# Kernel optimization log

Measured on AMD Instinct MI355X. Metric: run time of the kernel, lower is better.

The kernel has to match this reference:

```python
import jax, jax.numpy as jnp
import numpy as np

B, T, IN_DIM, OUT_DIM, H = 2, 256, 512, 256, 8
TEMP = 1.0
BN_EPS = 1e-5


def _boundary_mask(bnd):
    # bnd: (B, T) float in {0,1}. Vectorized version of the nested-loop
    # construction: mask[j,k] = prod_{m=min(j,k)..max(j,k)} (1 - bnd[m]), diag=1.
    q = 1.0 - bnd  # (B, T)
    ar = jnp.arange(T)

    def per_batch(qb):
        def row(j):
            # cumprod of q starting at position j (entries before j treated as 1)
            return jnp.cumprod(jnp.where(ar >= j, qb, 1.0))
        M = jax.vmap(row)(ar)                 # (T, T); valid for k >= j
        upper = ar[None, :] >= ar[:, None]
        full = jnp.where(upper, M, M.T)       # symmetrize
        eye = ar[None, :] == ar[:, None]
        return jnp.where(eye, 1.0, full)      # diagonal forced to 1

    return jax.vmap(per_batch)(q)             # (B, T, T)


def setup_inputs() -> dict:
    key = jax.random.key(0)
    ks = jax.random.split(key, 8)
    s_in = 1.0 / np.sqrt(IN_DIM)
    s_hin = 1.0 / np.sqrt(H * IN_DIM)
    return {
        "x": jax.random.normal(ks[0], (B, T, IN_DIM), dtype=jnp.float32),
        "boundary": jax.random.randint(ks[1], (B, T), 0, 2, dtype=jnp.int32),
        "att_proj_w": jax.random.normal(ks[2], (OUT_DIM, IN_DIM), dtype=jnp.float32) * s_in,
        "att_proj_b": jnp.zeros((OUT_DIM,), dtype=jnp.float32),
        "att_weight": jax.random.normal(ks[3], (OUT_DIM, H), dtype=jnp.float32) * (1.0 / np.sqrt(OUT_DIM)),
        "proj_att_w": jax.random.normal(ks[4], (OUT_DIM, H * IN_DIM), dtype=jnp.float32) * s_hin,
        "proj_att_b": jnp.zeros((OUT_DIM,), dtype=jnp.float32),
        "proj_noatt_w": jax.random.normal(ks[5], (OUT_DIM, IN_DIM), dtype=jnp.float32) * s_in,
        "proj_noatt_b": jnp.zeros((OUT_DIM,), dtype=jnp.float32),
        "bn_gamma": jnp.ones((OUT_DIM,), dtype=jnp.float32),
        "bn_beta": jnp.zeros((OUT_DIM,), dtype=jnp.float32),
    }


def reference(x, boundary, att_proj_w, att_proj_b, att_weight,
              proj_att_w, proj_att_b, proj_noatt_w, proj_noatt_b,
              bn_gamma, bn_beta):
    bnd = boundary.astype(x.dtype)

    # pairwise node products: (B, T, T, IN_DIM)
    pm = x[:, :, None, :] * x[:, None, :, :]
    # attention logits: tanh(Linear) @ att_weight -> (B, T, T, H)
    a = jnp.tanh(jnp.einsum('bjkd,od->bjko', pm, att_proj_w) + att_proj_b)
    att = jnp.einsum('bjko,oh->bjkh', a, att_weight) / TEMP

    # boundary message-control mask, then softmax over the key-node axis (dim=-2)
    mask = _boundary_mask(bnd)                 # (B, T, T)
    att = att * mask[..., None]
    att = jax.nn.softmax(att, axis=-2)

    # aggregate per head; torch flattens (IN_DIM, H) -> IN_DIM*H with d-major order
    x1 = jnp.einsum('bjkh,bkd->bjdh', att, x).reshape(x.shape[0], x.shape[1], -1)
    x1 = x1 @ proj_att_w.T + proj_att_b
    x2 = x @ proj_noatt_w.T + proj_noatt_b
    y = x1 + x2                                # (B, T, OUT_DIM)

    # BatchNorm1d in training mode over flattened (B*T, OUT_DIM), biased variance
    flat = y.reshape(-1, y.shape[-1])
    mu = flat.mean(axis=0)
    var = flat.var(axis=0)
    yn = (flat - mu) * jax.lax.rsqrt(var + BN_EPS) * bn_gamma + bn_beta
    return jax.nn.selu(yn.reshape(y.shape))
```

## Files before the change

### kernel.cpp

```cpp
#include <hip/hip_runtime.h>
#include <hip/hip_bf16.h>

#define B_ 2
#define T_ 256
#define D_ 512
#define O_ 256
#define H_ 8

typedef __attribute__((ext_vector_type(4))) float f32x4;
typedef __attribute__((ext_vector_type(8))) short bf16x8;
typedef unsigned short u16;
typedef unsigned int u32;

__device__ __forceinline__ u16 f2b(float f) {
    u32 u = __builtin_bit_cast(u32, f);
    u32 r = (u + 0x7FFFu + ((u >> 16) & 1u)) >> 16;
    return (u16)r;
}
__device__ __forceinline__ u32 cvtpk(float lo, float hi) {
    u32 r;
    asm("v_cvt_pk_bf16_f32 %0, %1, %2" : "=v"(r) : "v"(lo), "v"(hi));
    return r;
}
__device__ __forceinline__ float fast_tanh(float x) {
    float ax = fabsf(x);
    float e = __expf(-2.f * ax);
    float r = (1.f - e) / (1.f + e);
    return x < 0.f ? -r : r;
}
__device__ __forceinline__ uint4 ld8f2b(const float* __restrict__ p) {
    f32x4 a = *reinterpret_cast<const f32x4*>(p);
    f32x4 b = *reinterpret_cast<const f32x4*>(p + 4);
    uint4 pk;
    pk.x = cvtpk(a[0], a[1]);
    pk.y = cvtpk(a[2], a[3]);
    pk.z = cvtpk(b[0], b[1]);
    pk.w = cvtpk(b[2], b[3]);
    return pk;
}
__device__ __forceinline__ void gload16(const void* g, void* l) {
    __builtin_amdgcn_global_load_lds(
        (const __attribute__((address_space(1))) unsigned int*)g,
        (__attribute__((address_space(3))) unsigned int*)l, 16, 0, 0);
}

__global__ void k0_prep(const float* __restrict__ x, const float* __restrict__ W2,
                        const int* __restrict__ bnd,
                        u16* __restrict__ Xbf, u16* __restrict__ W2t,
                        int* __restrict__ scan_g) {
    const int tid = threadIdx.x;
    if (blockIdx.x < 64) {
        int base = (blockIdx.x * 256 + tid) * 16;
        uint4 o0 = ld8f2b(x + base);
        uint4 o1 = ld8f2b(x + base + 8);
        *reinterpret_cast<uint4*>(Xbf + base) = o0;
        *reinterpret_cast<uint4*>(Xbf + base + 8) = o1;
        return;
    }
    if (blockIdx.x >= 192) {
        const int b = blockIdx.x - 192;
        __shared__ int sc[256];
        sc[tid] = bnd[b * 256 + tid];
        __syncthreads();
        for (int off = 1; off < 256; off <<= 1) {
            int v = (tid >= off) ? sc[tid - off] : 0;
            __syncthreads();
            sc[tid] += v;
            __syncthreads();
        }
        scan_g[b * 256 + tid] = sc[tid];
        return;
    }
    const int bx2 = blockIdx.x - 64;
    const int o0 = (bx2 >> 3) * 16;
    const int dc = bx2 & 7;
    __shared__ u16 TL[8192];
    #pragma unroll
    for (int c = 0; c < 8; ++c) {
        int i = tid * 32 + c * 4;
        int r = i >> 9, rem = i & 511;
        f32x4 v = *reinterpret_cast<const f32x4*>(
            W2 + (size_t)(o0 + r) * 4096 + dc * 512 + rem);
        int dd = rem >> 3, h0 = rem & 7;
        TL[(h0 + 0) * 1024 + r * 64 + dd] = f2b(v[0]);
        TL[(h0 + 1) * 1024 + r * 64 + dd] = f2b(v[1]);
        TL[(h0 + 2) * 1024 + r * 64 + dd] = f2b(v[2]);
        TL[(h0 + 3) * 1024 + r * 64 + dd] = f2b(v[3]);
    }
    __syncthreads();
    #pragma unroll
    for (int c = 0; c < 4; ++c) {
        int jj = tid * 32 + c * 8;
        int h = jj >> 10, r = (jj >> 6) & 15, dd = jj & 63;
        *reinterpret_cast<uint4*>(W2t + (size_t)(h * 256 + o0 + r) * 512 + dc * 64 + dd) =
            *reinterpret_cast<const uint4*>(&TL[jj]);
    }
}

__launch_bounds__(256, 4)
__global__ void k1a_att(const u16* __restrict__ Xbf, const float* __restrict__ xf,
                        const float* __restrict__ Wap, const float* __restrict__ bap,
                        const float* __restrict__ aw, float* __restrict__ attpart)
{
    const int oc = blockIdx.x & 3;
    const int j = (blockIdx.x >> 2) & 255;
    const int b = blockIdx.x >> 10;
    const int jt = j >> 6;
    const int tid = threadIdx.x;
    const int w = tid >> 6;
    const int l = tid & 63;
    const int l15 = l & 15;
    const int lgp = l >> 4;
    const bool act = (w >= jt);

    __shared__ __align__(16) u16 XL[256 * 64];
    __shared__ __align__(16) u16 WL[64 * 64];

    const u16* xb = Xbf + b * (T_ * D_);
    const float* xjp = xf + (b * T_ + j) * D_;

    bf16x8 bwreg[2];
    #pragma unroll
    for (int ds = 0; ds < 2; ++ds) {
        u16 awtmp[8];
        #pragma unroll
        for (int e = 0; e < 8; ++e)
            awtmp[e] = (l15 < 8) ? f2b(aw[(oc * 64 + ds * 32 + lgp * 8 + e) * 8 + l15]) : (u16)0;
        bwreg[ds] = *reinterpret_cast<const bf16x8*>(awtmp);
    }

    const int srow_off = (l >> 3);
    const int scol = ((l & 7) ^ ((l >> 3) & 7)) * 8;
    const int i0 = jt * 2;
    const int wr0 = tid >> 3, wsc = (tid & 7) * 8;
    const int wswz0 = ((tid & 7) ^ (wr0 & 7)) * 8;

    f32x4 acc[4][4] = {};
    for (int d0 = 0; d0 < D_; d0 += 64) {
        __syncthreads();
        #pragma unroll
        for (int i = 0; i < 8; ++i) {
            if (i >= i0) {
                int row = i * 32 + w * 8 + srow_off;
                gload16(xb + row * 512 + d0 + scol, &XL[i * 2048 + w * 512]);
            }
        }
        {
            f32x4 xa = *reinterpret_cast<const f32x4*>(xjp + d0 + wsc);
            f32x4 xc = *reinterpret_cast<const f32x4*>(xjp + d0 + wsc + 4);
            const float* wp0 = Wap + (size_t)(oc * 64 + wr0) * 512 + d0 + wsc;
            f32x4 va = *reinterpret_cast<const f32x4*>(wp0);
            f32x4 vb = *reinterpret_cast<const f32x4*>(wp0 + 4);
            uint4 pk;
            pk.x = cvtpk(va[0] * xa[0], va[1] * xa[1]);
            pk.y = cvtpk(va[2] * xa[2], va[3] * xa[3]);
            pk.z = cvtpk(vb[0] * xc[0], vb[1] * xc[1]);
            pk.w = cvtpk(vb[2] * xc[2], vb[3] * xc[3]);
            *reinterpret_cast<uint4*>(&WL[wr0 * 64 + wswz0]) = pk;
            const float* wp1 = wp0 + 32 * 512;
            va = *reinterpret_cast<const f32x4*>(wp1);
            vb = *reinterpret_cast<const f32x4*>(wp1 + 4);
            pk.x = cvtpk(va[0] * xa[0], va[1] * xa[1]);
            pk.y = cvtpk(va[2] * xa[2], va[3] * xa[3]);
            pk.z = cvtpk(vb[0] * xc[0], vb[1] * xc[1]);
            pk.w = cvtpk(vb[2] * xc[2], vb[3] * xc[3]);
            *reinterpret_cast<uint4*>(&WL[(wr0 + 32) * 64 + wswz0]) = pk;
        }
        __syncthreads();
        if (act) {
            #pragma unroll
            for (int ds = 0; ds < 2; ++ds) {
                bf16x8 wfr[4];
                #pragma unroll
                for (int ot = 0; ot < 4; ++ot) {
                    int wc = ((ds * 4 + lgp) ^ (l15 & 7)) * 8;
                    wfr[ot] = *reinterpret_cast<const bf16x8*>(&WL[(ot * 16 + l15) * 64 + wc]);
                }
                #pragma unroll
                for (int kt = 0; kt < 4; ++kt) {
                    int row = w * 64 + kt * 16 + l15;
                    int c16 = ((ds * 4 + lgp) ^ (l15 & 7)) * 8;
                    bf16x8 xfr = *reinterpret_cast<const bf16x8*>(&XL[row * 64 + c16]);
                    #pragma unroll
                    for (int ot = 0; ot < 4; ++ot)
                        acc[ot][kt] = __builtin_amdgcn_mfma_f32_16x16x32_bf16(wfr[ot], xfr, acc[ot][kt], 0, 0, 0);
                }
            }
        }
    }
    u16* a_lds = XL;
    if (act) {
        #pragma unroll
        for (int ot = 0; ot < 4; ++ot) {
            f32x4 bv = *reinterpret_cast<const f32x4*>(bap + oc * 64 + ot * 16 + lgp * 4);
            #pragma unroll
            for (int kt = 0; kt < 4; ++kt) {
                int k = w * 64 + kt * 16 + l15;
                float t0 = fast_tanh(acc[ot][kt][0] + bv[0]);
                float t1 = fast_tanh(acc[ot][kt][1] + bv[1]);
                float t2 = fast_tanh(acc[ot][kt][2] + bv[2]);
                float t3 = fast_tanh(acc[ot][kt][3] + bv[3]);
                uint2 pk;
                pk.x = cvtpk(t0, t1);
                pk.y = cvtpk(t2, t3);
                int c16 = (ot * 2 + (lgp >> 1)) ^ (l15 & 7);
                *reinterpret_cast<uint2*>(&a_lds[k * 64 + c16 * 8 + (lgp & 1) * 4]) = pk;
            }
        }
    }
    f32x4 attacc[4] = {};
    if (act) {
        #pragma unroll
        for (int ds = 0; ds < 2; ++ds) {
            #pragma unroll
            for (int kt = 0; kt < 4; ++kt) {
                int row = w * 64 + kt * 16 + l15;
                int c16 = ((ds * 4 + lgp) ^ (l15 & 7)) * 8;
                bf16x8 af = *reinterpret_cast<const bf16x8*>(&a_lds[row * 64 + c16]);
                attacc[kt] = __builtin_amdgcn_mfma_f32_16x16x32_bf16(af, bwreg[ds], attacc[kt], 0, 0, 0);
            }
        }
        float* dst = attpart + ((size_t)blockIdx.x) * 256 * 8;
        #pragma unroll
        for (int kt = 0; kt < 4; ++kt) {
            if (l15 < 8) {
                #pragma unroll
                for (int i = 0; i < 4; ++i) {
                    int k = w * 64 + kt * 16 + lgp * 4 + i;
                    dst[k * 8 + l15] = attacc[kt][i];
                }
            }
        }
        if (w > jt && l15 < 8) {
            #pragma unroll
            for (int kt = 0; kt < 4; ++kt) {
                #pragma unroll
                for (int i = 0; i < 4; ++i) {
                    int k = w * 64 + kt * 16 + lgp * 4 + i;
                    attpart[(((size_t)(b * 256 + k)) * 4 + oc) * 2048 + j * 8 + l15] = attacc[kt][i];
                }
            }
        }
    }
}

__global__ void k1b_sm(const float* __restrict__ attpart, const int* __restrict__ scan_g,
                       u16* __restrict__ P2)
{
    const int b = blockIdx.x >> 8;
    const int j = blockIdx.x & 255;
    const int tid = threadIdx.x;

    __shared__ float attL[256 * 9];
    __shared__ float maskv[256];

    {
        int k = tid;
        const int* sg = scan_g + b * 256;
        float m;
        if (k == j) m = 1.f;
        else if (k > j) m = ((sg[k] - (j ? sg[j - 1] : 0)) == 0) ? 1.f : 0.f;
        else m = ((sg[j] - (k ? sg[k - 1] : 0)) == 0) ? 1.f : 0.f;
        maskv[k] = m;
    }
    {
        const float* base = attpart + ((size_t)(b * 256 + j) * 4) * 256 * 8 + tid * 8;
        f32x4 s0 = *reinterpret_cast<const f32x4*>(base);
        f32x4 s1 = *reinterpret_cast<const f32x4*>(base + 4);
        #pragma unroll
        for (int oc = 1; oc < 4; ++oc) {
            s0 += *reinterpret_cast<const f32x4*>(base + (size_t)oc * 2048);
            s1 += *reinterpret_cast<const f32x4*>(base + (size_t)oc * 2048 + 4);
        }
        #pragma unroll
        for (int e = 0; e < 4; ++e) attL[tid * 9 + e] = s0[e];
        #pragma unroll
        for (int e = 0; e < 4; ++e) attL[tid * 9 + 4 + e] = s1[e];
    }
    __syncthreads();

    {
        int h = tid >> 5, c = tid & 31;
        float lgv[8];
        float mx = -3.4e38f;
        #pragma unroll
        for (int kk = 0; kk < 8; ++kk) {
            int k = c + kk * 32;
            float v = attL[k * 9 + h] * maskv[k];
            lgv[kk] = v;
            mx = fmaxf(mx, v);
        }
        #pragma unroll
        for (int off = 1; off < 32; off <<= 1)
            mx = fmaxf(mx, __shfl_xor(mx, off, 32));
        float sum = 0.f;
        #pragma unroll
        for (int kk = 0; kk < 8; ++kk) {
            lgv[kk] = __expf(lgv[kk] - mx);
            sum += lgv[kk];
        }
        #pragma unroll
        for (int off = 1; off < 32; off <<= 1)
            sum += __shfl_xor(sum, off, 32);
        float inv = 1.f / sum;
        u16* dst = P2 + ((size_t)(b * 256 + j)) * 2048 + h * 256;
        #pragma unroll
        for (int kk = 0; kk < 8; ++kk)
            dst[c + kk * 32] = f2b(lgv[kk] * inv);
    }
}

__launch_bounds__(256, 4)
__global__ void k2m_mm(const u16* __restrict__ Xbf, const u16* __restrict__ W2t,
                       u16* __restrict__ M)
{
    const int kh = blockIdx.x & 1;
    const int on = (blockIdx.x >> 1) & 15;
    const int h = (blockIdx.x >> 5) & 7;
    const int b = blockIdx.x >> 8;
    const int tid = threadIdx.x;
    const int w = tid >> 6, l = tid & 63, l15 = l & 15, lgp = l >> 4;

    __shared__ __align__(16) u16 XL[128 * 64];
    __shared__ __align__(16) u16 WL[16 * 72];

    const u16* xb = Xbf + b * (T_ * D_) + kh * 128 * D_;
    const int srow_off = (l >> 3);
    const int scol = ((l & 7) ^ ((l >> 3) & 7)) * 8;

    f32x4 acc[2] = {};
    for (int d0 = 0; d0 < D_; d0 += 64) {
        __syncthreads();
        #pragma unroll
        for (int i = 0; i < 4; ++i) {
            int row = i * 32 + w * 8 + srow_off;
            gload16(xb + row * 512 + d0 + scol, &XL[i * 2048 + w * 512]);
        }
        if (tid < 128) {
            int r = tid >> 3, s = tid & 7;
            *reinterpret_cast<uint4*>(&WL[r * 72 + s * 8]) =
                *reinterpret_cast<const uint4*>(
                    W2t + (size_t)(h * 256 + on * 16 + r) * 512 + d0 + s * 8);
        }
        __syncthreads();
        #pragma unroll
        for (int ds = 0; ds < 2; ++ds) {
            bf16x8 bfr = *reinterpret_cast<const bf16x8*>(&WL[l15 * 72 + ds * 32 + lgp * 8]);
            #pragma unroll
            for (int kt = 0; kt < 2; ++kt) {
                int row = w * 32 + kt * 16 + l15;
                int c16 = ((ds * 4 + lgp) ^ (l15 & 7)) * 8;
                bf16x8 afr = *reinterpret_cast<const bf16x8*>(&XL[row * 64 + c16]);
                acc[kt] = __builtin_amdgcn_mfma_f32_16x16x32_bf16(afr, bfr, acc[kt], 0, 0, 0);
            }
        }
    }
    u16* dst = M + ((size_t)(b * 8 + h) * 256 + on * 16 + l15) * 256 + kh * 128;
    #pragma unroll
    for (int kt = 0; kt < 2; ++kt) {
        uint2 pk;
        pk.x = cvtpk(acc[kt][0], acc[kt][1]);
        pk.y = cvtpk(acc[kt][2], acc[kt][3]);
        *reinterpret_cast<uint2*>(dst + w * 32 + kt * 16 + lgp * 4) = pk;
    }
}

__launch_bounds__(256, 4)
__global__ void k3_mm(const u16* __restrict__ P2, const u16* __restrict__ M,
                      const u16* __restrict__ Xbf, const float* __restrict__ W3,
                      float* __restrict__ part)
{
    const int gid = blockIdx.x;
    const int tid = threadIdx.x;
    const int w = tid >> 6, l = tid & 63, l15 = l & 15, lgp = l >> 4;

    __shared__ __align__(16) u16 AL[64 * 72];
    __shared__ __align__(16) u16 BL[64 * 72];

    f32x4 acc[4] = {};
    int jc, oc, slot;
    if (gid < 128) {
        int kc = gid & 3;
        oc = (gid >> 2) & 3;
        jc = gid >> 4;
        slot = kc;
        const int j0 = jc * 64, o0 = oc * 64;
        const int bb = jc >> 2;
        for (int t = 0; t < 8; ++t) {
            const int hh = kc * 2 + (t >> 2);
            const int k0 = (t & 3) * 64;
            __syncthreads();
            #pragma unroll
            for (int c = 0; c < 2; ++c) {
                int cc = tid + c * 256;
                int r = cc >> 3, s = cc & 7;
                *reinterpret_cast<uint4*>(&AL[r * 72 + s * 8]) =
                    *reinterpret_cast<const uint4*>(
                        P2 + (size_t)(j0 + r) * 2048 + hh * 256 + k0 + s * 8);
                *reinterpret_cast<uint4*>(&BL[r * 72 + s * 8]) =
                    *reinterpret_cast<const uint4*>(
                        M + ((size_t)(bb * 8 + hh) * 256 + o0 + r) * 256 + k0 + s * 8);
            }
            __syncthreads();
            #pragma unroll
            for (int ds = 0; ds < 2; ++ds) {
                bf16x8 afr = *reinterpret_cast<const bf16x8*>(&AL[(w * 16 + l15) * 72 + ds * 32 + lgp * 8]);
                #pragma unroll
                for (int ot = 0; ot < 4; ++ot) {
                    bf16x8 bfr = *reinterpret_cast<const bf16x8*>(&BL[(ot * 16 + l15) * 72 + ds * 32 + lgp * 8]);
                    acc[ot] = __builtin_amdgcn_mfma_f32_16x16x32_bf16(afr, bfr, acc[ot], 0, 0, 0);
                }
            }
        }
    } else {
        int g2 = gid - 128;
        oc = g2 & 3;
        jc = g2 >> 2;
        slot = 4;
        const int j0 = jc * 64, o0 = oc * 64;
        for (int t0 = 0; t0 < 512; t0 += 64) {
            __syncthreads();
            #pragma unroll
            for (int c = 0; c < 2; ++c) {
                int cc = tid + c * 256;
                int r = cc >> 3, s = cc & 7;
                *reinterpret_cast<uint4*>(&AL[r * 72 + s * 8]) =
                    *reinterpret_cast<const uint4*>(Xbf + (size_t)(j0 + r) * 512 + t0 + s * 8);
                *reinterpret_cast<uint4*>(&BL[r * 72 + s * 8]) =
                    ld8f2b(W3 + (size_t)(o0 + r) * 512 + t0 + s * 8);
            }
            __syncthreads();
            #pragma unroll
            for (int ds = 0; ds < 2; ++ds) {
                bf16x8 afr = *reinterpret_cast<const bf16x8*>(&AL[(w * 16 + l15) * 72 + ds * 32 + lgp * 8]);
                #pragma unroll
                for (int ot = 0; ot < 4; ++ot) {
                    bf16x8 bfr = *reinterpret_cast<const bf16x8*>(&BL[(ot * 16 + l15) * 72 + ds * 32 + lgp * 8]);
                    acc[ot] = __builtin_amdgcn_mfma_f32_16x16x32_bf16(afr, bfr, acc[ot], 0, 0, 0);
                }
            }
        }
    }
    const int j0 = jc * 64, o0 = oc * 64;
    float* dst = part + (size_t)slot * 512 * 256;
    #pragma unroll
    for (int ot = 0; ot < 4; ++ot)
        #pragma unroll
        for (int i = 0; i < 4; ++i) {
            int rr = j0 + w * 16 + lgp * 4 + i;
            int o = o0 + ot * 16 + l15;
            dst[rr * 256 + o] = acc[ot][i];
        }
}

__global__ void k4a_comb(const float* __restrict__ part,
                         const float* __restrict__ pb2, const float* __restrict__ pb3,
                         float* __restrict__ ypre,
                         float* __restrict__ psum, float* __restrict__ psq)
{
    int g = blockIdx.x, o = threadIdx.x;
    float bsum = pb2[o] + pb3[o];
    float s = 0.f, q = 0.f;
    for (int r = g * 8; r < g * 8 + 8; ++r) {
        size_t idx = (size_t)r * 256 + o;
        float v = part[idx] + part[131072 + idx] + part[2 * 131072 + idx]
                + part[3 * 131072 + idx] + part[4 * 131072 + idx] + bsum;
        ypre[idx] = v;
        s += v; q += v * v;
    }
    psum[g * 256 + o] = s;
    psq[g * 256 + o] = q;
}

__global__ void k4b_norm(const float* __restrict__ ypre,
                         const float* __restrict__ psum, const float* __restrict__ psq,
                         const float* __restrict__ gamma, const float* __restrict__ beta,
                         float* __restrict__ out) {
    int r = blockIdx.x, o = threadIdx.x;
    float s = 0.f, q = 0.f;
    #pragma unroll 8
    for (int g = 0; g < 64; ++g) {
        s += psum[g * 256 + o];
        q += psq[g * 256 + o];
    }
    float mu = s * (1.f / 512.f);
    float var = q * (1.f / 512.f) - mu * mu;
    float inv = rsqrtf(var + 1e-5f);
    float v = (ypre[r * 256 + o] - mu) * inv * gamma[o] + beta[o];
    const float SC = 1.0507009873554805f, AL = 1.6732632423543772f;
    float ov = v > 0.f ? SC * v : SC * AL * (__expf(v) - 1.f);
    out[r * 256 + o] = ov;
}

extern "C" void kernel_launch(void* const* d_in, const int* in_sizes, int n_in,
                              void* d_out, int out_size, void* d_ws, size_t ws_size,
                              hipStream_t stream) {
    const float* x    = (const float*)d_in[0];
    const int* bnd    = (const int*)d_in[1];
    const float* Wap  = (const float*)d_in[2];
    const float* bap  = (const float*)d_in[3];
    const float* aw   = (const float*)d_in[4];
    const float* W2   = (const float*)d_in[5];
    const float* pb2  = (const float*)d_in[6];
    const float* W3   = (const float*)d_in[7];
    const float* pb3  = (const float*)d_in[8];
    const float* gamma = (const float*)d_in[9];
    const float* beta  = (const float*)d_in[10];
    float* out = (float*)d_out;
    (void)in_sizes; (void)n_in; (void)out_size; (void)ws_size;

    char* ws = (char*)d_ws;
    u16* Xbf   = (u16*)ws;  ws += (size_t)B_ * T_ * D_ * 2;
    u16* W2t   = (u16*)ws;  ws += (size_t)H_ * O_ * D_ * 2;
    u16* P2    = (u16*)ws;  ws += (size_t)B_ * T_ * H_ * T_ * 2;
    u16* Mbuf  = (u16*)ws;  ws += (size_t)B_ * H_ * O_ * T_ * 2;
    float* part = (float*)ws; ws += (size_t)5 * 512 * 256 * 4;
    float* ypre = (float*)ws; ws += (size_t)B_ * T_ * O_ * 4;
    float* psum = (float*)ws; ws += (size_t)64 * O_ * 4;
    float* psq  = (float*)ws; ws += (size_t)64 * O_ * 4;
    int* scan_g = (int*)ws;  ws += (size_t)B_ * T_ * 4;
    float* attpart = (float*)ws; ws += (size_t)2048 * 256 * 8 * 4;

    k0_prep<<<194, 256, 0, stream>>>(x, W2, bnd, Xbf, W2t, scan_g);
    k1a_att<<<2048, 256, 0, stream>>>(Xbf, x, Wap, bap, aw, attpart);
    k1b_sm<<<512, 256, 0, stream>>>(attpart, scan_g, P2);
    k2m_mm<<<512, 256, 0, stream>>>(Xbf, W2t, Mbuf);
    k3_mm<<<160, 256, 0, stream>>>(P2, Mbuf, Xbf, W3, part);
    k4a_comb<<<64, 256, 0, stream>>>(part, pb2, pb3, ypre, psum, psq);
    k4b_norm<<<512, 256, 0, stream>>>(ypre, psum, psq, gamma, beta, out);
}
```

Measured before the change: 88.74 us.

## Process two output chunks per block in attention-logit kernel with 512 threads

Each k1a_att block now handles two of the four 64-wide output chunks instead of one and uses 8 waves of 32 key rows each. Each X tile loaded into LDS is therefore reused across two W chunks, halving X tile traffic and the block count. The cost is larger blocks with more accumulator registers per wave and a second WL buffer in LDS, which may lower occupancy. The attpart write indexing is rewritten to address by (b, j, oc).

New measurement: 114.0 us. +28.5%, slower.

```diff
diff --git a/kernel.cpp b/kernel.cpp
--- a/kernel.cpp
+++ b/kernel.cpp
@@ -97,93 +97,93 @@
     }
 }
 
-__launch_bounds__(256, 4)
+__launch_bounds__(512, 4)
 __global__ void k1a_att(const u16* __restrict__ Xbf, const float* __restrict__ xf,
                         const float* __restrict__ Wap, const float* __restrict__ bap,
                         const float* __restrict__ aw, float* __restrict__ attpart)
 {
-    const int oc = blockIdx.x & 3;
-    const int j = (blockIdx.x >> 2) & 255;
-    const int b = blockIdx.x >> 10;
+    const int op = blockIdx.x & 1;
+    const int j = (blockIdx.x >> 1) & 255;
+    const int b = blockIdx.x >> 9;
     const int jt = j >> 6;
     const int tid = threadIdx.x;
     const int w = tid >> 6;
     const int l = tid & 63;
     const int l15 = l & 15;
     const int lgp = l >> 4;
-    const bool act = (w >= jt);
+    const bool act = (w >= jt * 2);
 
     __shared__ __align__(16) u16 XL[256 * 64];
-    __shared__ __align__(16) u16 WL[64 * 64];
+    __shared__ __align__(16) u16 WL[2][64 * 64];
 
     const u16* xb = Xbf + b * (T_ * D_);
     const float* xjp = xf + (b * T_ + j) * D_;
 
-    bf16x8 bwreg[2];
+    bf16x8 bwreg[2][2];
     #pragma unroll
-    for (int ds = 0; ds < 2; ++ds) {
-        u16 awtmp[8];
-        #pragma unroll
-        for (int e = 0; e < 8; ++e)
-            awtmp[e] = (l15 < 8) ? f2b(aw[(oc * 64 + ds * 32 + lgp * 8 + e) * 8 + l15]) : (u16)0;
-        bwreg[ds] = *reinterpret_cast<const bf16x8*>(awtmp);
-    }
+    for (int pc = 0; pc < 2; ++pc)
+        #pragma unroll
+        for (int ds = 0; ds < 2; ++ds) {
+            u16 awtmp[8];
+            #pragma unroll
+            for (int e = 0; e < 8; ++e)
+                awtmp[e] = (l15 < 8)
+                    ? f2b(aw[((op * 2 + pc) * 64 + ds * 32 + lgp * 8 + e) * 8 + l15])
+                    : (u16)0;
+            bwreg[pc][ds] = *reinterpret_cast<const bf16x8*>(awtmp);
+        }
 
     const int srow_off = (l >> 3);
     const int scol = ((l & 7) ^ ((l >> 3) & 7)) * 8;
-    const int i0 = jt * 2;
-    const int wr0 = tid >> 3, wsc = (tid & 7) * 8;
-    const int wswz0 = ((tid & 7) ^ (wr0 & 7)) * 8;
-
-    f32x4 acc[4][4] = {};
+    const int wr = tid >> 3, wsc = (tid & 7) * 8;
+    const int wswz = ((tid & 7) ^ (wr & 7)) * 8;
+
+    f32x4 acc[2][4][2] = {};
     for (int d0 = 0; d0 < D_; d0 += 64) {
         __syncthreads();
-        #pragma unroll
-        for (int i = 0; i < 8; ++i) {
-            if (i >= i0) {
-                int row = i * 32 + w * 8 + srow_off;
-                gload16(xb + row * 512 + d0 + scol, &XL[i * 2048 + w * 512]);
+        if (act) {
+            #pragma unroll
+            for (int i = 0; i < 4; ++i) {
+                int row = w * 32 + i * 8 + srow_off;
+                gload16(xb + row * 512 + d0 + scol, &XL[w * 2048 + i * 512]);
             }
         }
         {
             f32x4 xa = *reinterpret_cast<const f32x4*>(xjp + d0 + wsc);
             f32x4 xc = *reinterpret_cast<const f32x4*>(xjp + d0 + wsc + 4);
-            const float* wp0 = Wap + (size_t)(oc * 64 + wr0) * 512 + d0 + wsc;
-            f32x4 va = *reinterpret_cast<const f32x4*>(wp0);
-            f32x4 vb = *reinterpret_cast<const f32x4*>(wp0 + 4);
-            uint4 pk;
-            pk.x = cvtpk(va[0] * xa[0], va[1] * xa[1]);
-            pk.y = cvtpk(va[2] * xa[2], va[3] * xa[3]);
-            pk.z = cvtpk(vb[0] * xc[0], vb[1] * xc[1]);
-            pk.w = cvtpk(vb[2] * xc[2], vb[3] * xc[3]);
-            *reinterpret_cast<uint4*>(&WL[wr0 * 64 + wswz0]) = pk;
-            const float* wp1 = wp0 + 32 * 512;
-            va = *reinterpret_cast<const f32x4*>(wp1);
-            vb = *reinterpret_cast<const f32x4*>(wp1 + 4);
-            pk.x = cvtpk(va[0] * xa[0], va[1] * xa[1]);
-            pk.y = cvtpk(va[2] * xa[2], va[3] * xa[3]);
-            pk.z = cvtpk(vb[0] * xc[0], vb[1] * xc[1]);
-            pk.w = cvtpk(vb[2] * xc[2], vb[3] * xc[3]);
-            *reinterpret_cast<uint4*>(&WL[(wr0 + 32) * 64 + wswz0]) = pk;
+            #pragma unroll
+            for (int pc = 0; pc < 2; ++pc) {
+                const float* wp = Wap + (size_t)((op * 2 + pc) * 64 + wr) * 512 + d0 + wsc;
+                f32x4 va = *reinterpret_cast<const f32x4*>(wp);
+                f32x4 vb = *reinterpret_cast<const f32x4*>(wp + 4);
+                uint4 pk;
+                pk.x = cvtpk(va[0] * xa[0], va[1] * xa[1]);
+                pk.y = cvtpk(va[2] * xa[2], va[3] * xa[3]);
+                pk.z = cvtpk(vb[0] * xc[0], vb[1] * xc[1]);
+                pk.w = cvtpk(vb[2] * xc[2], vb[3] * xc[3]);
+                *reinterpret_cast<uint4*>(&WL[pc][wr * 64 + wswz]) = pk;
+            }
         }
         __syncthreads();
         if (act) {
             #pragma unroll
-            for (int ds = 0; ds < 2; ++ds) {
-                bf16x8 wfr[4];
+            for (int pc = 0; pc < 2; ++pc) {
                 #pragma unroll
-                for (int ot = 0; ot < 4; ++ot) {
+                for (int ds = 0; ds < 2; ++ds) {
                     int wc = ((ds * 4 + lgp) ^ (l15 & 7)) * 8;
-                    wfr[ot] = *reinterpret_cast<const bf16x8*>(&WL[(ot * 16 + l15) * 64 + wc]);
-                }
-                #pragma unroll
-                for (int kt = 0; kt < 4; ++kt) {
-                    int row = w * 64 + kt * 16 + l15;
-                    int c16 = ((ds * 4 + lgp) ^ (l15 & 7)) * 8;
-                    bf16x8 xfr = *reinterpret_cast<const bf16x8*>(&XL[row * 64 + c16]);
+                    bf16x8 wfr[4];
                     #pragma unroll
                     for (int ot = 0; ot < 4; ++ot)
-                        acc[ot][kt] = __builtin_amdgcn_mfma_f32_16x16x32_bf16(wfr[ot], xfr, acc[ot][kt], 0, 0, 0);
+                        wfr[ot] = *reinterpret_cast<const bf16x8*>(&WL[pc][(ot * 16 + l15) * 64 + wc]);
+                    #pragma unroll
+                    for (int kt = 0; kt < 2; ++kt) {
+                        int row = w * 32 + kt * 16 + l15;
+                        bf16x8 xfr = *reinterpret_cast<const bf16x8*>(&XL[row * 64 + wc]);
+                        #pragma unroll
+                        for (int ot = 0; ot < 4; ++ot)
+                            acc[pc][ot][kt] = __builtin_amdgcn_mfma_f32_16x16x32_bf16(
+                                wfr[ot], xfr, acc[pc][ot][kt], 0, 0, 0);
+                    }
                 }
             }
         }
@@ -191,53 +191,56 @@
     u16* a_lds = XL;
     if (act) {
         #pragma unroll
-        for (int ot = 0; ot < 4; ++ot) {
-            f32x4 bv = *reinterpret_cast<const f32x4*>(bap + oc * 64 + ot * 16 + lgp * 4);
-            #pragma unroll
-            for (int kt = 0; kt < 4; ++kt) {
-                int k = w * 64 + kt * 16 + l15;
-                float t0 = fast_tanh(acc[ot][kt][0] + bv[0]);
-                float t1 = fast_tanh(acc[ot][kt][1] + bv[1]);
-                float t2 = fast_tanh(acc[ot][kt][2] + bv[2]);
-                float t3 = fast_tanh(acc[ot][kt][3] + bv[3]);
-                uint2 pk;
-                pk.x = cvtpk(t0, t1);
-                pk.y = cvtpk(t2, t3);
-                int c16 = (ot * 2 + (lgp >> 1)) ^ (l15 & 7);
-                *reinterpret_cast<uint2*>(&a_lds[k * 64 + c16 * 8 + (lgp & 1) * 4]) = pk;
-            }
-        }
-    }
-    f32x4 attacc[4] = {};
-    if (act) {
-        #pragma unroll
-        for (int ds = 0; ds < 2; ++ds) {
-            #pragma unroll
-            for (int kt = 0; kt < 4; ++kt) {
-                int row = w * 64 + kt * 16 + l15;
-                int c16 = ((ds * 4 + lgp) ^ (l15 & 7)) * 8;
-                bf16x8 af = *reinterpret_cast<const bf16x8*>(&a_lds[row * 64 + c16]);
-                attacc[kt] = __builtin_amdgcn_mfma_f32_16x16x32_bf16(af, bwreg[ds], attacc[kt], 0, 0, 0);
-            }
-        }
-        float* dst = attpart + ((size_t)blockIdx.x) * 256 * 8;
-        #pragma unroll
-        for (int kt = 0; kt < 4; ++kt) {
-            if (l15 < 8) {
+        for (int pc = 0; pc < 2; ++pc) {
+            const int oc = op * 2 + pc;
+            #pragma unroll
+            for (int ot = 0; ot < 4; ++ot) {
+                f32x4 bv = *reinterpret_cast<const f32x4*>(bap + oc * 64 + ot * 16 + lgp * 4);
                 #pragma unroll
-                for (int i = 0; i < 4; ++i) {
-                    int k = w * 64 + kt * 16 + lgp * 4 + i;
-                    dst[k * 8 + l15] = attacc[kt][i];
-                }
-            }
-        }
-        if (w > jt && l15 < 8) {
-            #pragma unroll
-            for (int kt = 0; kt < 4; ++kt) {
+                for (int kt = 0; kt < 2; ++kt) {
+                    int k = w * 32 + kt * 16 + l15;
+                    float t0 = fast_tanh(acc[pc][ot][kt][0] + bv[0]);
+                    float t1 = fast_tanh(acc[pc][ot][kt][1] + bv[1]);
+                    float t2 = fast_tanh(acc[pc][ot][kt][2] + bv[2]);
+                    float t3 = fast_tanh(acc[pc][ot][kt][3] + bv[3]);
+                    uint2 pk;
+                    pk.x = cvtpk(t0, t1);
+                    pk.y = cvtpk(t2, t3);
+                    int c16 = (ot * 2 + (lgp >> 1)) ^ (l15 & 7);
+                    *reinterpret_cast<uint2*>(&a_lds[k * 64 + c16 * 8 + (lgp & 1) * 4]) = pk;
+                }
+            }
+            f32x4 attacc[2] = {};
+            #pragma unroll
+            for (int ds = 0; ds < 2; ++ds) {
                 #pragma unroll
-                for (int i = 0; i < 4; ++i) {
-                    int k = w * 64 + kt * 16 + lgp * 4 + i;
-                    attpart[(((size_t)(b * 256 + k)) * 4 + oc) * 2048 + j * 8 + l15] = attacc[kt][i];
+                for (int kt = 0; kt < 2; ++kt) {
+                    int row = w * 32 + kt * 16 + l15;
+                    int c16 = ((ds * 4 + lgp) ^ (l15 & 7)) * 8;
+                    bf16x8 af = *reinterpret_cast<const bf16x8*>(&a_lds[row * 64 + c16]);
+                    attacc[kt] = __builtin_amdgcn_mfma_f32_16x16x32_bf16(
+                        af, bwreg[pc][ds], attacc[kt], 0, 0, 0);
+                }
+            }
+            float* dst = attpart + (((size_t)(b * 256 + j)) * 4 + oc) * 2048;
+            #pragma unroll
+            for (int kt = 0; kt < 2; ++kt) {
+                if (l15 < 8) {
+                    #pragma unroll
+                    for (int i = 0; i < 4; ++i) {
+                        int k = w * 32 + kt * 16 + lgp * 4 + i;
+                        dst[k * 8 + l15] = attacc[kt][i];
+                    }
+                }
+            }
+            if ((w >> 1) > jt && l15 < 8) {
+                #pragma unroll
+                for (int kt = 0; kt < 2; ++kt) {
+                    #pragma unroll
+                    for (int i = 0; i < 4; ++i) {
+                        int k = w * 32 + kt * 16 + lgp * 4 + i;
+                        attpart[(((size_t)(b * 256 + k)) * 4 + oc) * 2048 + j * 8 + l15] = attacc[kt][i];
+                    }
                 }
             }
         }
@@ -522,7 +525,7 @@
     float* attpart = (float*)ws; ws += (size_t)2048 * 256 * 8 * 4;
 
     k0_prep<<<194, 256, 0, stream>>>(x, W2, bnd, Xbf, W2t, scan_g);
-    k1a_att<<<2048, 256, 0, stream>>>(Xbf, x, Wap, bap, aw, attpart);
+    k1a_att<<<1024, 512, 0, stream>>>(Xbf, x, Wap, bap, aw, attpart);
     k1b_sm<<<512, 256, 0, stream>>>(attpart, scan_g, P2);
     k2m_mm<<<512, 256, 0, stream>>>(Xbf, W2t, Mbuf);
     k3_mm<<<160, 256, 0, stream>>>(P2, Mbuf, Xbf, W3, part);
```
